# Optimization experiments

Measured on AMD Instinct MI355X. Metric: run time of the kernel, lower is better.

The kernel has to match this reference:

```python
import jax, jax.numpy as jnp
import numpy as np

JOINTS = 17
SKELETON = ((1, 2), (0, 1), (0, 2), (2, 4), (1, 3), (6, 8), (8, 10), (5, 7), (7, 9),
            (12, 14), (14, 16), (11, 13), (13, 15), (5, 6), (11, 12), (5, 11), (6, 12),
            (3, 5), (4, 6))
DIM = 512
HEADS = 8
HEAD_DIM = DIM // HEADS
SCALE = HEAD_DIM ** -0.5
ON = 64           # obj_emb seq len; HEADS*ON must equal 512 (size of W)
HIDDEN = 4 * DIM
BN_EPS = 1e-5
LN_EPS = 1e-5


def make_adj():
    a = np.eye(JOINTS, dtype=np.float32)
    for i, j in SKELETON:
        a[i, j] = 1.0
        a[j, i] = 1.0
    return jnp.asarray(a)


def layer_norm(x, w, b):
    mu = jnp.mean(x, axis=-1, keepdims=True)
    var = jnp.var(x, axis=-1, keepdims=True)
    return (x - mu) * jax.lax.rsqrt(var + LN_EPS) * w + b


def setup_inputs() -> dict:
    key = jax.random.key(0)
    ks = jax.random.split(key, 12)
    B = 2048
    inp = {
        "noise": jax.random.normal(ks[0], (B, JOINTS, DIM), jnp.float32),
        "obj_emb": jax.random.normal(ks[1], (B, ON, DIM), jnp.float32),
        "ln1_w": jnp.ones((DIM,), jnp.float32),
        "ln1_b": jnp.zeros((DIM,), jnp.float32),
        "ln2_w": jnp.ones((DIM,), jnp.float32),
        "ln2_b": jnp.zeros((DIM,), jnp.float32),
        "q_w": jax.random.normal(ks[2], (DIM, DIM), jnp.float32) * 0.02,
        "kv_w": jax.random.normal(ks[3], (2 * DIM, DIM), jnp.float32) * 0.02,
        "W": jax.random.normal(ks[4], (HEADS * ON, HEADS * ON), jnp.float32) * 0.001,
        "bn_g": jnp.ones((HEADS * ON,), jnp.float32),
        "bn_b": jnp.zeros((HEADS * ON,), jnp.float32),
        "proj_w": jax.random.normal(ks[5], (DIM, DIM), jnp.float32) * 0.02,
        "proj_b": jnp.zeros((DIM,), jnp.float32),
        "fc1_w": jax.random.normal(ks[6], (HIDDEN, DIM), jnp.float32) * 0.02,
        "fc1_b": jnp.zeros((HIDDEN,), jnp.float32),
        "fc2_w": jax.random.normal(ks[7], (DIM, HIDDEN), jnp.float32) * 0.02,
        "fc2_b": jnp.zeros((DIM,), jnp.float32),
    }
    return inp


def reference(noise, obj_emb, ln1_w, ln1_b, ln2_w, ln2_b, q_w, kv_w, W,
              bn_g, bn_b, proj_w, proj_b, fc1_w, fc1_b, fc2_w, fc2_b):
    B = noise.shape[0]
    adj = make_adj()

    # --- attention branch (norm1 applied to both inputs with same params) ---
    x1 = layer_norm(noise, ln1_w, ln1_b)          # [B,17,C]
    e1 = layer_norm(obj_emb, ln1_w, ln1_b)        # [B,64,C]

    q = (x1 @ q_w.T).reshape(B, JOINTS, HEADS, HEAD_DIM).transpose(0, 2, 1, 3)  # [B,H,17,hd]
    kv = (e1 @ kv_w.T).reshape(B, ON, 2, HEADS, HEAD_DIM).transpose(2, 0, 3, 1, 4)
    k, v = kv[0], kv[1]                            # [B,H,64,hd]

    attn = jnp.einsum('bhnd,bhmd->bhnm', q, k) * SCALE        # [B,H,17,64]
    attn = attn.transpose(0, 2, 1, 3).reshape(B, JOINTS, HEADS * ON)  # [B,17,512]
    attn = attn @ W                                            # [B,17,512]

    # BatchNorm1d (training mode): stats over B*17 rows, biased variance
    flat = attn.reshape(B * JOINTS, HEADS * ON)
    mu = jnp.mean(flat, axis=0)
    var = jnp.var(flat, axis=0)
    flat = (flat - mu) * jax.lax.rsqrt(var + BN_EPS) * bn_g + bn_b
    attn = flat.reshape(B, JOINTS, HEADS * ON)

    attn = jnp.einsum('ij,bjk->bik', adj, attn)               # adjacency bmm
    attn = attn.reshape(B, JOINTS, HEADS, ON).transpose(0, 2, 1, 3)  # [B,H,17,64]
    attn = jax.nn.softmax(attn, axis=-1)

    x = jnp.einsum('bhnm,bhmd->bhnd', attn, v)                # [B,H,17,hd]
    x = x.transpose(0, 2, 1, 3).reshape(B, JOINTS, DIM)
    x = x @ proj_w.T + proj_b

    x = noise + x

    # --- MLP branch ---
    y = layer_norm(x, ln2_w, ln2_b)
    y = jax.nn.gelu(y @ fc1_w.T + fc1_b, approximate=False)
    y = y @ fc2_w.T + fc2_b
    return x + y
```

## Files before the change

kernel.cpp:

```cpp
#include <hip/hip_runtime.h>
#include <math.h>

typedef unsigned short ushort_t;
typedef short short8 __attribute__((ext_vector_type(8)));
typedef float f32x4 __attribute__((ext_vector_type(4)));

#define MFMA16(a,b,c) __builtin_amdgcn_mfma_f32_16x16x32_bf16(a,b,c,0,0,0)

__device__ __forceinline__ ushort_t f2bf(float f){
  unsigned u = __builtin_bit_cast(unsigned, f);
  u += 0x7fffu + ((u >> 16) & 1u);
  return (ushort_t)(u >> 16);
}

__device__ __forceinline__ void gld16(const void* g, void* l){
  __builtin_amdgcn_global_load_lds(
      (const __attribute__((address_space(1))) void*)g,
      (__attribute__((address_space(3))) void*)l, 16, 0, 0);
}

__global__ __launch_bounds__(256)
void prep_weights(const float* __restrict__ q_w, const float* __restrict__ kv_w,
                  const float* __restrict__ proj_w, const float* __restrict__ fc1_w,
                  const float* __restrict__ fc2_w, const float* __restrict__ Wm,
                  const float* __restrict__ ln1w, const float* __restrict__ ln2w,
                  ushort_t* __restrict__ q_wb, ushort_t* __restrict__ kv_wb,
                  ushort_t* __restrict__ proj_wb, ushort_t* __restrict__ fc1_wb,
                  ushort_t* __restrict__ fc2_wb, ushort_t* __restrict__ Wt_b)
{
  int i = blockIdx.x*256 + threadIdx.x;
  if (i < 262144){
    q_wb[i] = f2bf(q_w[i] * ln1w[i & 511]);
  } else if (i < 786432){
    int j = i - 262144;
    kv_wb[j] = f2bf(kv_w[j] * ln1w[j & 511]);
  } else if (i < 1048576){
    int j = i - 786432;
    proj_wb[j] = f2bf(proj_w[j]);
  } else if (i < 2097152){
    int j = i - 1048576;
    fc1_wb[j] = f2bf(fc1_w[j] * ln2w[j & 511]);
  } else if (i < 3145728){
    int j = i - 2097152;
    fc2_wb[j] = f2bf(fc2_w[j]);
  } else if (i < 3407872){
    int j = i - 3145728;
    int n = j >> 9, k = j & 511;
    Wt_b[j] = f2bf(Wm[(k << 9) + n]);
  }
}

__global__ __launch_bounds__(64)
void prep_bias(const float* __restrict__ q_w, const float* __restrict__ kv_w,
               const float* __restrict__ fc1_w, const float* __restrict__ ln1b,
               const float* __restrict__ ln2b, const float* __restrict__ fc1_b,
               float* __restrict__ qbias, float* __restrict__ kvbias,
               float* __restrict__ fc1bias)
{
  int blk = blockIdx.x, lane = threadIdx.x;
  const float* w; const float* lnb; float* o; float base = 0.f; int n;
  if (blk < 512){ n = blk; w = q_w; lnb = ln1b; o = qbias; }
  else if (blk < 1536){ n = blk - 512; w = kv_w; lnb = ln1b; o = kvbias; }
  else { n = blk - 1536; w = fc1_w; lnb = ln2b; o = fc1bias; }
  float s = 0.f;
  for (int k = lane; k < 512; k += 64) s += w[(size_t)n*512 + k]*lnb[k];
  for (int m = 32; m; m >>= 1) s += __shfl_xor(s, m);
  if (lane == 0){
    if (blk >= 1536) base = fc1_b[n];
    o[n] = s + base;
  }
}

__global__ __launch_bounds__(256)
void lnorm(const float* __restrict__ X, ushort_t* __restrict__ O){
  int row = blockIdx.x*4 + (threadIdx.x >> 6);
  int lane = threadIdx.x & 63;
  const float4* p = (const float4*)(X + (size_t)row*512 + lane*8);
  float4 a = p[0], c = p[1];
  float s = a.x+a.y+a.z+a.w + c.x+c.y+c.z+c.w;
  float q = a.x*a.x+a.y*a.y+a.z*a.z+a.w*a.w + c.x*c.x+c.y*c.y+c.z*c.z+c.w*c.w;
  for (int m = 32; m; m >>= 1){ s += __shfl_xor(s, m); q += __shfl_xor(q, m); }
  float mn = s*(1.f/512.f);
  float rs = rsqrtf(q*(1.f/512.f) - mn*mn + 1e-5f);
  short8 pk;
  pk[0]=(short)f2bf((a.x-mn)*rs); pk[1]=(short)f2bf((a.y-mn)*rs);
  pk[2]=(short)f2bf((a.z-mn)*rs); pk[3]=(short)f2bf((a.w-mn)*rs);
  pk[4]=(short)f2bf((c.x-mn)*rs); pk[5]=(short)f2bf((c.y-mn)*rs);
  pk[6]=(short)f2bf((c.z-mn)*rs); pk[7]=(short)f2bf((c.w-mn)*rs);
  *(short8*)(O + (size_t)row*512 + lane*8) = pk;
}

template<int EPI>
__global__ __launch_bounds__(256)
void gemm_k(const ushort_t* __restrict__ A, const ushort_t* __restrict__ Bt,
            int M, int N, int K,
            const float* __restrict__ bias, const float* __restrict__ resid,
            void* __restrict__ out, void* __restrict__ out2)
{
  __shared__ __align__(16) ushort_t As[128*64];
  __shared__ __align__(16) ushort_t Bs[128*64];
  const int tid = threadIdx.x;
  const int wave = tid >> 6, lane = tid & 63;

  const int nwg = gridDim.x;
  const int qc = nwg >> 3, rc = nwg & 7;
  const int xcd = blockIdx.x & 7, sl = blockIdx.x >> 3;
  const int bid = (xcd < rc ? xcd*(qc+1) : rc*(qc+1) + (xcd-rc)*qc) + sl;

  const int tiles_n = N >> 7;
  const int tn = bid % tiles_n, tm = bid / tiles_n;
  const int wm = wave >> 1, wn = wave & 1;
  const int segr = lane >> 3;
  const int ksw  = ((lane & 7) ^ segr) * 8;

  f32x4 acc[4][4] = {};

  for (int kt = 0; kt < K; kt += 64){
    for (int i = 0; i < 4; i++){
      int seg = wave*4 + i;
      int row = seg*8 + segr;
      gld16(Bt + (size_t)(tn*128 + row)*K + kt + ksw, (void*)(Bs + seg*512));
      gld16(A  + (size_t)(tm*128 + row)*K + kt + ksw, (void*)(As + seg*512));
    }
    __syncthreads();
    for (int kk = 0; kk < 2; kk++){
      int kc = kk*32 + (lane >> 4)*8;
      short8 af[4], bfr[4];
      for (int mi = 0; mi < 4; mi++){
        int r = wm*64 + mi*16 + (lane & 15);
        af[mi] = *(const short8*)&As[r*64 + (kc ^ ((r & 7) << 3))];
      }
      for (int ni = 0; ni < 4; ni++){
        int r = wn*64 + ni*16 + (lane & 15);
        bfr[ni] = *(const short8*)&Bs[r*64 + (kc ^ ((r & 7) << 3))];
      }
      for (int mi = 0; mi < 4; mi++)
        for (int ni = 0; ni < 4; ni++)
          acc[mi][ni] = MFMA16(af[mi], bfr[ni], acc[mi][ni]);
    }
    __syncthreads();
  }

  for (int ni = 0; ni < 4; ni++){
    int col = tn*128 + wn*64 + ni*16 + (lane & 15);
    float bv = bias ? bias[col] : 0.f;
    for (int mi = 0; mi < 4; mi++){
      f32x4 v = acc[mi][ni];
      int row0 = tm*128 + wm*64 + mi*16 + (lane >> 4)*4;
      if constexpr (EPI == 4){
        if (col < 512){
          for (int j = 0; j < 4; j++){
            size_t idx = (size_t)(row0 + j)*512 + col;
            ((ushort_t*)out)[idx] = f2bf(v[j] + bv);
          }
        } else {
          int hh = (col - 512) >> 6, dd = (col - 512) & 63;
          int bb = row0 >> 6, mm0 = row0 & 63;
          ushort_t pk[4];
          for (int j = 0; j < 4; j++) pk[j] = f2bf(v[j] + bv);
          *(uint2*)((ushort_t*)out2 + ((((size_t)bb*8 + hh)*64 + dd) << 6) + mm0) =
              *(const uint2*)pk;
        }
      } else {
        for (int j = 0; j < 4; j++){
          int row = row0 + j;
          size_t idx = (size_t)row*N + col;
          float x = v[j] + bv;
          if constexpr (EPI == 0) ((ushort_t*)out)[idx] = f2bf(x);
          else if constexpr (EPI == 1) ((float*)out)[idx] = x;
          else if constexpr (EPI == 2) ((float*)out)[idx] = x + resid[idx];
          else if constexpr (EPI == 3){
            float g = 0.5f*x*(1.f + erff(x*0.70710678118f));
            ((ushort_t*)out)[idx] = f2bf(g);
          }
        }
      }
    }
  }
}

__global__ __launch_bounds__(256)
void qk_kernel(const ushort_t* __restrict__ Q, const ushort_t* __restrict__ Kb,
               ushort_t* __restrict__ S)
{
  int b = blockIdx.x;
  int wave = threadIdx.x >> 6, lane = threadIdx.x & 63;
  for (int h = wave; h < 8; h += 4){
    f32x4 acc[2][4] = {};
    for (int kk = 0; kk < 2; kk++){
      int kd = kk*32 + (lane >> 4)*8;
      short8 a[2], bb[4];
      for (int mi = 0; mi < 2; mi++){
        int n = mi*16 + (lane & 15); if (n > 16) n = 16;
        a[mi] = *(const short8*)&Q[((size_t)b*17 + n)*512 + h*64 + kd];
      }
      for (int ni = 0; ni < 4; ni++){
        int m = ni*16 + (lane & 15);
        bb[ni] = *(const short8*)&Kb[((size_t)b*64 + m)*512 + h*64 + kd];
      }
      for (int mi = 0; mi < 2; mi++)
        for (int ni = 0; ni < 4; ni++)
          acc[mi][ni] = MFMA16(a[mi], bb[ni], acc[mi][ni]);
    }
    for (int mi = 0; mi < 2; mi++)
      for (int ni = 0; ni < 4; ni++)
        for (int j = 0; j < 4; j++){
          int rr = mi*16 + (lane >> 4)*4 + j;
          if (rr < 17)
            S[((size_t)b*17 + rr)*512 + h*64 + ni*16 + (lane & 15)] =
                f2bf(acc[mi][ni][j]*0.125f);
        }
  }
}

__global__ __launch_bounds__(256)
void pv_kernel(const ushort_t* __restrict__ P, const ushort_t* __restrict__ Vt,
               ushort_t* __restrict__ X)
{
  int b = blockIdx.x;
  int wave = threadIdx.x >> 6, lane = threadIdx.x & 63;
  for (int h = wave; h < 8; h += 4){
    f32x4 acc[2][4] = {};
    for (int kk = 0; kk < 2; kk++){
      int km = kk*32 + (lane >> 4)*8;
      short8 a[2], bb[4];
      for (int mi = 0; mi < 2; mi++){
        int n = mi*16 + (lane & 15); if (n > 16) n = 16;
        a[mi] = *(const short8*)&P[((size_t)b*17 + n)*512 + h*64 + km];
      }
      for (int ni = 0; ni < 4; ni++){
        int d = ni*16 + (lane & 15);
        bb[ni] = *(const short8*)&Vt[(((size_t)b*8 + h)*64 + d)*64 + km];
      }
      for (int mi = 0; mi < 2; mi++)
        for (int ni = 0; ni < 4; ni++)
          acc[mi][ni] = MFMA16(a[mi], bb[ni], acc[mi][ni]);
    }
    for (int mi = 0; mi < 2; mi++)
      for (int ni = 0; ni < 4; ni++)
        for (int j = 0; j < 4; j++){
          int rr = mi*16 + (lane >> 4)*4 + j;
          if (rr < 17)
            X[((size_t)b*17 + rr)*512 + h*64 + ni*16 + (lane & 15)] =
                f2bf(acc[mi][ni][j]);
        }
  }
}

__global__ __launch_bounds__(256)
void bn_stats(const float* __restrict__ preBN, float* __restrict__ sums){
  int t = threadIdx.x;
  size_t base = (size_t)blockIdx.x * 256 * 512;
  int c0 = t, c1 = t + 256;
  float s0=0, q0=0, s1=0, q1=0;
  for (int r = 0; r < 256; r++){
    float a = preBN[base + (size_t)r*512 + c0];
    float b = preBN[base + (size_t)r*512 + c1];
    s0 += a; q0 += a*a; s1 += b; q1 += b*b;
  }
  atomicAdd(&sums[c0], s0);       atomicAdd(&sums[512 + c0], q0);
  atomicAdd(&sums[c1], s1);       atomicAdd(&sums[512 + c1], q1);
}

__global__ void bn_finalize(const float* __restrict__ sums, const float* __restrict__ g,
                            const float* __restrict__ b, float* __restrict__ scale,
                            float* __restrict__ shift, float invN){
  int c = blockIdx.x*256 + threadIdx.x;
  if (c < 512){
    float mean = sums[c]*invN;
    float var  = sums[512 + c]*invN - mean*mean;
    float sc = g[c]*rsqrtf(var + 1e-5f);
    scale[c] = sc; shift[c] = b[c] - mean*sc;
  }
}

__constant__ unsigned ADJM[17] = {
  0x7u, 0xFu, 0x17u, 0x2Au, 0x54u, 0x8E8u, 0x1170u, 0x2A0u, 0x540u,
  0x280u, 0x500u, 0x3820u, 0x5840u, 0xA800u, 0x15000u, 0xA000u, 0x14000u };

__global__ __launch_bounds__(256)
void bn_adj_softmax(const float* __restrict__ preBN, const float* __restrict__ scale,
                    const float* __restrict__ shift, ushort_t* __restrict__ Asm)
{
  __shared__ float yt[17*512];
  int b = blockIdx.x, tid = threadIdx.x;
  const float* src = preBN + (size_t)b*17*512;
  for (int i = tid; i < 17*512; i += 256){
    int c = i & 511;
    yt[i] = src[i]*scale[c] + shift[c];
  }
  __syncthreads();
  int qw = tid >> 4, l16 = tid & 15;
  for (int g = qw; g < 136; g += 16){
    int n = g >> 3, h = g & 7;
    float z[4];
    unsigned msk = ADJM[n];
    for (int u = 0; u < 4; u++){
      int c = h*64 + l16 + u*16;
      float sv = 0.f;
      unsigned mm = msk;
      while (mm){ int j = __ffs(mm) - 1; mm &= mm - 1; sv += yt[j*512 + c]; }
      z[u] = sv;
    }
    float mx = fmaxf(fmaxf(z[0], z[1]), fmaxf(z[2], z[3]));
    for (int m = 8; m; m >>= 1) mx = fmaxf(mx, __shfl_xor(mx, m, 16));
    float e0 = expf(z[0]-mx), e1 = expf(z[1]-mx), e2 = expf(z[2]-mx), e3 = expf(z[3]-mx);
    float ss = e0 + e1 + e2 + e3;
    for (int m = 8; m; m >>= 1) ss += __shfl_xor(ss, m, 16);
    float inv = 1.f/ss;
    size_t ob = ((size_t)b*17 + n)*512 + h*64 + l16;
    Asm[ob]      = f2bf(e0*inv);
    Asm[ob + 16] = f2bf(e1*inv);
    Asm[ob + 32] = f2bf(e2*inv);
    Asm[ob + 48] = f2bf(e3*inv);
  }
}

extern "C" void kernel_launch(void* const* d_in, const int* in_sizes, int n_in,
                              void* d_out, int out_size, void* d_ws, size_t ws_size,
                              hipStream_t stream)
{
  const float* noise  = (const float*)d_in[0];
  const float* obj    = (const float*)d_in[1];
  const float* ln1w   = (const float*)d_in[2];
  const float* ln1b   = (const float*)d_in[3];
  const float* ln2w   = (const float*)d_in[4];
  const float* ln2b   = (const float*)d_in[5];
  const float* q_w    = (const float*)d_in[6];
  const float* kv_w   = (const float*)d_in[7];
  const float* Wm     = (const float*)d_in[8];
  const float* bn_g   = (const float*)d_in[9];
  const float* bn_b   = (const float*)d_in[10];
  const float* proj_w = (const float*)d_in[11];
  const float* proj_b = (const float*)d_in[12];
  const float* fc1_w  = (const float*)d_in[13];
  const float* fc1_b  = (const float*)d_in[14];
  const float* fc2_w  = (const float*)d_in[15];
  const float* fc2_b  = (const float*)d_in[16];

  const int B  = in_sizes[0] / (17*512);
  const int M  = B*17;
  const int MO = B*64;

  const size_t MiB = 1ull << 20;
  char* ws = (char*)d_ws;

  ushort_t* q_wb    = (ushort_t*)(ws + 0*MiB);
  ushort_t* kv_wb   = (ushort_t*)(ws + 1*MiB);
  ushort_t* proj_wb = (ushort_t*)(ws + 2*MiB);
  ushort_t* fc1_wb  = (ushort_t*)(ws + 3*MiB);
  ushort_t* fc2_wb  = (ushort_t*)(ws + 5*MiB);
  ushort_t* Wt_b    = (ushort_t*)(ws + 7*MiB);
  float* qbias   = (float*)(ws + 7*MiB + 600*1024);
  float* kvbias  = qbias + 1024;
  float* fc1bias = kvbias + 1024;
  float* bnsum   = fc1bias + 2048;
  float* bnscale = bnsum + 1024;
  float* bnshift = bnscale + 512;

  char* R1 = ws + 8*MiB;
  char* R2 = ws + 136*MiB;
  char* R3 = ws + 264*MiB;

  ushort_t* e1b  = (ushort_t*)R1;
  ushort_t* Kb   = (ushort_t*)R2;
  ushort_t* Vtb  = (ushort_t*)R3;
  ushort_t* x1b  = (ushort_t*)R1;
  ushort_t* Qb   = (ushort_t*)(R1 + 35*MiB);
  ushort_t* Sb   = (ushort_t*)(R1 + 70*MiB);
  ushort_t* Asm  = (ushort_t*)R1;
  ushort_t* PVo  = (ushort_t*)(R1 + 35*MiB);
  float*    preBN = (float*)R2;
  float*    xres  = (float*)R2;
  ushort_t* yb   = (ushort_t*)(R2 + 69*MiB);
  ushort_t* h1   = (ushort_t*)(R2 + 104*MiB);
  float*    outp = (float*)d_out;

  hipMemsetAsync(bnsum, 0, 1024*4, stream);
  prep_weights<<<dim3(3407872/256), 256, 0, stream>>>(
      q_w, kv_w, proj_w, fc1_w, fc2_w, Wm, ln1w, ln2w,
      q_wb, kv_wb, proj_wb, fc1_wb, fc2_wb, Wt_b);
  prep_bias<<<dim3(3584), 64, 0, stream>>>(
      q_w, kv_w, fc1_w, ln1b, ln2b, fc1_b, qbias, kvbias, fc1bias);

  lnorm<<<dim3(MO/4), 256, 0, stream>>>(obj, e1b);
  gemm_k<4><<<dim3((MO/128)*(1024/128)), 256, 0, stream>>>(
      e1b, kv_wb, MO, 1024, 512, kvbias, nullptr, Kb, Vtb);
  lnorm<<<dim3(M/4), 256, 0, stream>>>(noise, x1b);
  gemm_k<0><<<dim3((M/128)*(512/128)), 256, 0, stream>>>(
      x1b, q_wb, M, 512, 512, qbias, nullptr, Qb, nullptr);
  qk_kernel<<<dim3(B), 256, 0, stream>>>(Qb, Kb, Sb);
  gemm_k<1><<<dim3((M/128)*(512/128)), 256, 0, stream>>>(
      Sb, Wt_b, M, 512, 512, nullptr, nullptr, preBN, nullptr);
  bn_stats<<<dim3(M/256), 256, 0, stream>>>(preBN, bnsum);
  bn_finalize<<<dim3(2), 256, 0, stream>>>(bnsum, bn_g, bn_b, bnscale, bnshift, 1.f/(float)M);
  bn_adj_softmax<<<dim3(B), 256, 0, stream>>>(preBN, bnscale, bnshift, Asm);
  pv_kernel<<<dim3(B), 256, 0, stream>>>(Asm, Vtb, PVo);
  gemm_k<2><<<dim3((M/128)*(512/128)), 256, 0, stream>>>(
      PVo, proj_wb, M, 512, 512, proj_b, noise, xres, nullptr);

  lnorm<<<dim3(M/4), 256, 0, stream>>>(xres, yb);
  gemm_k<3><<<dim3((M/128)*(2048/128)), 256, 0, stream>>>(
      yb, fc1_wb, M, 2048, 512, fc1bias, nullptr, h1, nullptr);
  gemm_k<2><<<dim3((M/128)*(512/128)), 256, 0, stream>>>(
      h1, fc2_wb, M, 512, 2048, fc2_b, xres, outp, nullptr);
}
```

Before: 990.2 us.

## Replace GEMM with 256-row tiles and triple-buffered async LDS pipeline

Replaces the 128x128 single-buffered GEMM with a 512-thread kernel that uses 256xBN tiles (BN 128 or 256) and a 3-slot LDS ring. Global-to-LDS loads for step s+2 are issued while MFMAs run on step s, with explicit vmcnt waits, and the compute section gets raised wave priority. The goal is to hide global-load latency, cut the per-K-step barrier stalls, and raise data reuse per tile. In exchange it uses more LDS and registers per block, and launches fewer blocks on the smaller GEMMs, which can leave CUs underused.

```diff
diff --git a/kernel.cpp b/kernel.cpp
--- a/kernel.cpp
+++ b/kernel.cpp
@@ -90,63 +90,116 @@
   *(short8*)(O + (size_t)row*512 + lane*8) = pk;
 }
 
-template<int EPI>
-__global__ __launch_bounds__(256)
-void gemm_k(const ushort_t* __restrict__ A, const ushort_t* __restrict__ Bt,
-            int M, int N, int K,
-            const float* __restrict__ bias, const float* __restrict__ resid,
-            void* __restrict__ out, void* __restrict__ out2)
-{
-  __shared__ __align__(16) ushort_t As[128*64];
-  __shared__ __align__(16) ushort_t Bs[128*64];
-  const int tid = threadIdx.x;
+template<int BN, int EPI>
+__global__ __launch_bounds__(512, 2)
+void gemm256(const ushort_t* __restrict__ A, const ushort_t* __restrict__ Bt,
+             int M, int N, int K,
+             const float* __restrict__ bias, const float* __restrict__ resid,
+             void* __restrict__ out, void* __restrict__ out2)
+{
+  constexpr int NR    = BN / 64;
+  constexpr int ASLOT = 256 * 32;
+  constexpr int BSLOT = BN * 32;
+  constexpr int SLOT  = ASLOT + BSLOT;
+  __shared__ __align__(16) ushort_t lds[3 * SLOT];
+
+  const int tid  = threadIdx.x;
   const int wave = tid >> 6, lane = tid & 63;
+  const int wm   = wave >> 2, wn = wave & 3;
+  const int l15  = lane & 15, lq = lane >> 4;
 
   const int nwg = gridDim.x;
   const int qc = nwg >> 3, rc = nwg & 7;
   const int xcd = blockIdx.x & 7, sl = blockIdx.x >> 3;
   const int bid = (xcd < rc ? xcd*(qc+1) : rc*(qc+1) + (xcd-rc)*qc) + sl;
 
-  const int tiles_n = N >> 7;
+  const int tiles_n = N / BN;
   const int tn = bid % tiles_n, tm = bid / tiles_n;
-  const int wm = wave >> 1, wn = wave & 1;
-  const int segr = lane >> 3;
-  const int ksw  = ((lane & 7) ^ segr) * 8;
-
-  f32x4 acc[4][4] = {};
-
-  for (int kt = 0; kt < K; kt += 64){
-    for (int i = 0; i < 4; i++){
-      int seg = wave*4 + i;
-      int row = seg*8 + segr;
-      gld16(Bt + (size_t)(tn*128 + row)*K + kt + ksw, (void*)(Bs + seg*512));
-      gld16(A  + (size_t)(tm*128 + row)*K + kt + ksw, (void*)(As + seg*512));
-    }
-    __syncthreads();
-    for (int kk = 0; kk < 2; kk++){
-      int kc = kk*32 + (lane >> 4)*8;
-      short8 af[4], bfr[4];
-      for (int mi = 0; mi < 4; mi++){
-        int r = wm*64 + mi*16 + (lane & 15);
-        af[mi] = *(const short8*)&As[r*64 + (kc ^ ((r & 7) << 3))];
-      }
-      for (int ni = 0; ni < 4; ni++){
-        int r = wn*64 + ni*16 + (lane & 15);
-        bfr[ni] = *(const short8*)&Bs[r*64 + (kc ^ ((r & 7) << 3))];
-      }
-      for (int mi = 0; mi < 4; mi++)
-        for (int ni = 0; ni < 4; ni++)
-          acc[mi][ni] = MFMA16(af[mi], bfr[ni], acc[mi][ni]);
-    }
-    __syncthreads();
-  }
-
-  for (int ni = 0; ni < 4; ni++){
-    int col = tn*128 + wn*64 + ni*16 + (lane & 15);
+  const int tileM = tm * 256, tileN = tn * BN;
+
+  const int gsw = (((tid & 3) - ((tid >> 3) & 3)) & 3) * 8;
+  const int srow = tid >> 2;
+
+  int offA[8], offB[NR];
+#pragma unroll
+  for (int mi = 0; mi < 8; mi++){
+    int r = wm*128 + mi*16 + l15;
+    offA[mi] = r*32 + (((lq + (r >> 1)) & 3) * 8);
+  }
+#pragma unroll
+  for (int ni = 0; ni < NR; ni++){
+    int r = wn*(BN/4) + ni*16 + l15;
+    offB[ni] = ASLOT + r*32 + (((lq + (r >> 1)) & 3) * 8);
+  }
+
+  f32x4 acc[8][NR] = {};
+
+  const int NT = K >> 5;
+
+  auto stage = [&](int step, int slot){
+    ushort_t* base = lds + slot * SLOT;
+    const int k0 = step * 32 + gsw;
+#pragma unroll
+    for (int i = 0; i < 2; i++)
+      gld16(A + (size_t)(tileM + i*128 + srow)*K + k0,
+            base + i*4096 + wave*512);
+#pragma unroll
+    for (int i = 0; i < BN/128; i++)
+      gld16(Bt + (size_t)(tileN + i*128 + srow)*K + k0,
+            base + ASLOT + i*4096 + wave*512);
+  };
+
+  stage(0, 0);
+  stage(1, 1);
+  if constexpr (BN == 256) asm volatile("s_waitcnt vmcnt(4)" ::: "memory");
+  else                     asm volatile("s_waitcnt vmcnt(3)" ::: "memory");
+  __builtin_amdgcn_sched_barrier(0);
+  __builtin_amdgcn_s_barrier();
+
+  int rs = 0;
+  for (int s = 0; s < NT; ++s){
+    const ushort_t* sb = lds + rs * SLOT;
+    short8 bfr[NR];
+#pragma unroll
+    for (int ni = 0; ni < NR; ni++)
+      bfr[ni] = *(const short8*)(sb + offB[ni]);
+
+    const bool more = (s + 2 < NT);
+    if (more){
+      int r2 = rs + 2; if (r2 >= 3) r2 -= 3;
+      stage(s + 2, r2);
+    }
+
+    __builtin_amdgcn_s_setprio(1);
+#pragma unroll
+    for (int mi = 0; mi < 8; mi++){
+      short8 af = *(const short8*)(sb + offA[mi]);
+#pragma unroll
+      for (int ni = 0; ni < NR; ni++)
+        acc[mi][ni] = MFMA16(af, bfr[ni], acc[mi][ni]);
+    }
+    __builtin_amdgcn_s_setprio(0);
+
+    if (more){
+      if constexpr (BN == 256) asm volatile("s_waitcnt vmcnt(4)" ::: "memory");
+      else                     asm volatile("s_waitcnt vmcnt(3)" ::: "memory");
+    } else {
+      asm volatile("s_waitcnt vmcnt(0)" ::: "memory");
+    }
+    __builtin_amdgcn_sched_barrier(0);
+    __builtin_amdgcn_s_barrier();
+
+    rs = (rs == 2) ? 0 : rs + 1;
+  }
+
+#pragma unroll
+  for (int ni = 0; ni < NR; ni++){
+    int col = tileN + wn*(BN/4) + ni*16 + l15;
     float bv = bias ? bias[col] : 0.f;
-    for (int mi = 0; mi < 4; mi++){
+#pragma unroll
+    for (int mi = 0; mi < 8; mi++){
       f32x4 v = acc[mi][ni];
-      int row0 = tm*128 + wm*64 + mi*16 + (lane >> 4)*4;
+      int row0 = tileM + wm*128 + mi*16 + lq*4;
       if constexpr (EPI == 4){
         if (col < 512){
           for (int j = 0; j < 4; j++){
@@ -384,24 +437,24 @@
       q_w, kv_w, fc1_w, ln1b, ln2b, fc1_b, qbias, kvbias, fc1bias);
 
   lnorm<<<dim3(MO/4), 256, 0, stream>>>(obj, e1b);
-  gemm_k<4><<<dim3((MO/128)*(1024/128)), 256, 0, stream>>>(
+  gemm256<256,4><<<dim3((MO/256)*(1024/256)), 512, 0, stream>>>(
       e1b, kv_wb, MO, 1024, 512, kvbias, nullptr, Kb, Vtb);
   lnorm<<<dim3(M/4), 256, 0, stream>>>(noise, x1b);
-  gemm_k<0><<<dim3((M/128)*(512/128)), 256, 0, stream>>>(
+  gemm256<128,0><<<dim3((M/256)*(512/128)), 512, 0, stream>>>(
       x1b, q_wb, M, 512, 512, qbias, nullptr, Qb, nullptr);
   qk_kernel<<<dim3(B), 256, 0, stream>>>(Qb, Kb, Sb);
-  gemm_k<1><<<dim3((M/128)*(512/128)), 256, 0, stream>>>(
+  gemm256<128,1><<<dim3((M/256)*(512/128)), 512, 0, stream>>>(
       Sb, Wt_b, M, 512, 512, nullptr, nullptr, preBN, nullptr);
   bn_stats<<<dim3(M/256), 256, 0, stream>>>(preBN, bnsum);
   bn_finalize<<<dim3(2), 256, 0, stream>>>(bnsum, bn_g, bn_b, bnscale, bnshift, 1.f/(float)M);
   bn_adj_softmax<<<dim3(B), 256, 0, stream>>>(preBN, bnscale, bnshift, Asm);
   pv_kernel<<<dim3(B), 256, 0, stream>>>(Asm, Vtb, PVo);
-  gemm_k<2><<<dim3((M/128)*(512/128)), 256, 0, stream>>>(
+  gemm256<128,2><<<dim3((M/256)*(512/128)), 512, 0, stream>>>(
       PVo, proj_wb, M, 512, 512, proj_b, noise, xres, nullptr);
 
   lnorm<<<dim3(M/4), 256, 0, stream>>>(xres, yb);
-  gemm_k<3><<<dim3((M/128)*(2048/128)), 256, 0, stream>>>(
+  gemm256<256,3><<<dim3((M/256)*(2048/256)), 512, 0, stream>>>(
       yb, fc1_wb, M, 2048, 512, fc1bias, nullptr, h1, nullptr);
-  gemm_k<2><<<dim3((M/128)*(512/128)), 256, 0, stream>>>(
+  gemm256<128,2><<<dim3((M/256)*(512/128)), 512, 0, stream>>>(
       h1, fc2_wb, M, 512, 2048, fc2_b, xres, outp, nullptr);
 }
```

Result: slower. 1.045 ms (+5.6%).
